# Kernel optimization log

Hardware: AMD Instinct MI355X
Metric: run time of the kernel (lower is better)

Reference implementation:

```python
import jax, jax.numpy as jnp
import numpy as np
from jax import lax

RF, NLF, MESH, FUSION = 64, 16, 16, 64


def _conv3x3(x, w, b):
    # stride 1, pad 1, ksize 3 == SAME
    y = lax.conv_general_dilated(x, w, (1, 1), 'SAME',
                                 dimension_numbers=('NCHW', 'OIHW', 'NCHW'))
    return y + b[None, :, None, None]


def _bn(x, g, b, m, v, eps=1e-5):
    scale = g / jnp.sqrt(v + eps)
    return (x - m[None, :, None, None]) * scale[None, :, None, None] + b[None, :, None, None]


def _rct_block(x, w1, b1, g, be, m, v, w2, b2):
    # extra_conv=True: Conv -> BN -> SiLU -> Conv (all stride 1)
    h = jax.nn.silu(_bn(_conv3x3(x, w1, b1), g, be, m, v))
    return _conv3x3(h, w2, b2)


def setup_inputs():
    key = jax.random.key(0)
    ks = jax.random.split(key, 8)
    B, H, W = 4, 512, 512
    return {
        'feature': jax.random.normal(ks[0], (B, RF, H, W), jnp.float32),
        'p_low': jax.random.normal(ks[1], (B, FUSION, MESH + 1, MESH + 1), jnp.float32),
        'r_w1': jax.random.normal(ks[2], (FUSION, FUSION, 3, 3), jnp.float32) * 0.05,
        'r_b1': jnp.zeros((FUSION,), jnp.float32),
        'r_gamma': jnp.ones((FUSION,), jnp.float32),
        'r_beta': jnp.zeros((FUSION,), jnp.float32),
        'r_mean': jnp.zeros((FUSION,), jnp.float32),
        'r_var': jnp.ones((FUSION,), jnp.float32),
        'r_w2': jax.random.normal(ks[3], (RF * NLF, FUSION, 3, 3), jnp.float32) * 0.05,
        'r_b2': jnp.zeros((RF * NLF,), jnp.float32),
        't_w1': jax.random.normal(ks[4], (FUSION, FUSION, 3, 3), jnp.float32) * 0.05,
        't_b1': jnp.zeros((FUSION,), jnp.float32),
        't_gamma': jnp.ones((FUSION,), jnp.float32),
        't_beta': jnp.zeros((FUSION,), jnp.float32),
        't_mean': jnp.zeros((FUSION,), jnp.float32),
        't_var': jnp.ones((FUSION,), jnp.float32),
        't_w2': jax.random.normal(ks[5], (3 * NLF, FUSION, 3, 3), jnp.float32) * 0.05,
        't_b2': jnp.zeros((3 * NLF,), jnp.float32),
    }


def reference(feature, p_low, r_w1, r_b1, r_gamma, r_beta, r_mean, r_var, r_w2, r_b2,
              t_w1, t_b1, t_gamma, t_beta, t_mean, t_var, t_w2, t_b2):
    B, C, H, W = feature.shape
    M = MESH
    mh, mw = H // M, W // M  # H,W divisible by mesh_size -> pad_tensor is identity
    P = mh * mw

    r_l = _rct_block(p_low, r_w1, r_b1, r_gamma, r_beta, r_mean, r_var, r_w2, r_b2)  # [B, RF*NLF, M+1, M+1]
    t_l = _rct_block(p_low, t_w1, t_b1, t_gamma, t_beta, t_mean, t_var, t_w2, t_b2)  # [B, 3*NLF, M+1, M+1]

    # channel dim factors as (feat, nlf); corners concat along nlf axis in order
    # (i,j), (i,j+1), (i+1,j), (i+1,j+1) -> K = 4*NLF keys per tile
    rc = r_l.reshape(B, RF, NLF, M + 1, M + 1)
    rk = jnp.concatenate([rc[..., :M, :M], rc[..., :M, 1:],
                          rc[..., 1:, :M], rc[..., 1:, 1:]], axis=2)  # [B,RF,4NLF,M,M]
    tc = t_l.reshape(B, 3, NLF, M + 1, M + 1)
    tk = jnp.concatenate([tc[..., :M, :M], tc[..., :M, 1:],
                          tc[..., 1:, :M], tc[..., 1:, 1:]], axis=2)  # [B,3,4NLF,M,M]

    # split feature into tiles: [B, M, M, P, RF] (row-major pixel order within tile)
    f = feature.reshape(B, RF, M, mh, M, mw).transpose(0, 2, 4, 3, 5, 1).reshape(B, M, M, P, RF)

    scale = 1.0 / jnp.sqrt(jnp.float32(RF))
    att = jnp.einsum('bxypr,brkxy->bxypk', f, rk) * scale  # [B,M,M,P,4NLF]
    att = jax.nn.softmax(att, axis=-1)
    out = jnp.einsum('bxypk,bckxy->bxycp', att, tk)  # [B,M,M,3,P]

    Y = out.reshape(B, M, M, 3, mh, mw).transpose(0, 3, 1, 4, 2, 5).reshape(B, 3, H, W)
    return Y
```

## Files before the change

### kernel.cpp

```cpp
#include <hip/hip_runtime.h>

typedef unsigned short u16;
typedef __bf16 bf16x8 __attribute__((ext_vector_type(8)));
typedef unsigned short us8 __attribute__((ext_vector_type(8)));
typedef float f32x4 __attribute__((ext_vector_type(4)));
typedef float f32x2 __attribute__((ext_vector_type(2)));
typedef unsigned int u32x4 __attribute__((ext_vector_type(4)));

union U8u { us8 s; u16 u[8]; };

__device__ __forceinline__ u16 f2bf(float f){
  unsigned u = __builtin_bit_cast(unsigned, f);
  u += 0x7fffu + ((u >> 16) & 1u);
  return (u16)(u >> 16);
}
__device__ __forceinline__ bf16x8 asbf(us8 x){ return __builtin_bit_cast(bf16x8, x); }

#define MFMA16(a,b,c) __builtin_amdgcn_mfma_f32_16x16x32_bf16((a),(b),(c),0,0,0)

__device__ __forceinline__ void stage_zero2(u16* sS, int tid){
  uint* z = (uint*)sS;
  for (int i = tid; i < 12996; i += 256) z[i] = 0u;
}

__device__ __forceinline__ void stage_src_f32T(const float* __restrict__ src,
                                               u16* sS, int tid){
  for (int i4 = tid; i4 < 4624; i4 += 256){
    int e = i4 * 4;
    f32x4 dv = *(const f32x4*)(src + e);
    #pragma unroll
    for (int t = 0; t < 4; t++){
      int ee = e + t;
      int ci = ee / 289; int rr = ee - ci*289;
      int oy = rr / 17;  int ox = rr - oy*17;
      sS[((oy+1)*19 + ox+1)*72 + ci] = f2bf(dv[t]);
    }
  }
}

__device__ __forceinline__ void stage_src_pm(const u16* __restrict__ src,
                                             u16* sS, int tid){
  for (int i8 = tid; i8 < 2312; i8 += 256){
    int pix = i8 >> 3, c0 = (i8 & 7) << 3;
    us8 v = *(const us8*)(src + ((size_t)pix << 6) + c0);
    int oy = pix / 17, ox = pix - oy*17;
    *(us8*)(sS + ((oy+1)*19 + ox+1)*72 + c0) = v;
  }
}

__device__ __forceinline__ void stage_w_f32(const float* __restrict__ w, int m0,
                                            u16* sW, int tid){
  for (int i4 = tid; i4 < 2304; i4 += 256){
    int e = i4 * 4;
    int co = e / 576; int r0 = e - co*576;
    f32x4 wv = *(const f32x4*)(w + (size_t)(m0+co)*576 + r0);
    #pragma unroll
    for (int t = 0; t < 4; t++){
      int r = r0 + t; int cin = r / 9; int tap = r - cin*9;
      sW[co*584 + tap*64 + cin] = f2bf(wv[t]);
    }
  }
}

__device__ __forceinline__ f32x4 conv_tile2(const u16* sS, const u16* sW,
                                            int nt, int l15, int q)
{
  int p = nt*16 + l15; int pc = p > 288 ? 288 : p;
  int oy = pc / 17, ox = pc - oy*17;
  f32x4 acc = {0.f, 0.f, 0.f, 0.f};
  #pragma unroll
  for (int ks = 0; ks < 18; ks++){
    const int tap = ks >> 1;
    const int dy = tap / 3, dx = tap - dy*3;
    int pix2 = (oy+dy)*19 + (ox+dx);
    us8 bv = *(const us8*)(sS + pix2*72 + (ks & 1)*32 + q*8);
    us8 av = *(const us8*)(sW + l15*584 + ks*32 + q*8);
    acc = MFMA16(asbf(av), asbf(bv), acc);
  }
  return acc;
}

__global__ __launch_bounds__(256) void conv1_k(
    const float* __restrict__ p_low,
    const float* __restrict__ wR, const float* __restrict__ b1R,
    const float* __restrict__ gR, const float* __restrict__ beR,
    const float* __restrict__ mR, const float* __restrict__ vR,
    const float* __restrict__ wT, const float* __restrict__ b1T,
    const float* __restrict__ gT, const float* __restrict__ beT,
    const float* __restrict__ mT, const float* __restrict__ vT,
    u16* __restrict__ hR, u16* __restrict__ hT)
{
  __shared__ __attribute__((aligned(16))) u16 sS[25992];
  __shared__ __attribute__((aligned(16))) u16 sW[9344];
  int tid = threadIdx.x;
  int bx = blockIdx.x;
  int job = bx >> 6;
  int b = (bx >> 4) & 3;
  int m0 = ((bx >> 2) & 3) << 4;
  int px = bx & 3;
  int nt0 = px * 5, ntEnd = nt0 + 5 > 19 ? 19 : nt0 + 5;
  const float* w  = job ? wT  : wR;
  const float* b1 = job ? b1T : b1R;
  const float* g  = job ? gT  : gR;
  const float* be = job ? beT : beR;
  const float* mn = job ? mT  : mR;
  const float* vr = job ? vT  : vR;
  u16* out = job ? hT : hR;
  const float* src = p_low + (size_t)b * 18496;

  stage_zero2(sS, tid);
  __syncthreads();
  stage_src_f32T(src, sS, tid);
  stage_w_f32(w, m0, sW, tid);
  __syncthreads();

  int lane = tid & 63, wave = tid >> 6;
  int l15 = lane & 15, q = lane >> 4;
  float scl[4], sft[4];
  #pragma unroll
  for (int e = 0; e < 4; e++){
    int co = m0 + q*4 + e;
    float s = g[co] / sqrtf(vr[co] + 1e-5f);
    scl[e] = s;
    sft[e] = (b1[co] - mn[co]) * s + be[co];
  }
  for (int nt = nt0 + wave; nt < ntEnd; nt += 4){
    f32x4 acc = conv_tile2(sS, sW, nt, l15, q);
    int p = nt*16 + l15;
    if (p < 289){
      float si[4];
      #pragma unroll
      for (int e = 0; e < 4; e++){
        float y = acc[e]*scl[e] + sft[e];
        si[e] = y / (1.f + __expf(-y));
      }
      uint2 pk;
      pk.x = (uint)f2bf(si[0]) | ((uint)f2bf(si[1]) << 16);
      pk.y = (uint)f2bf(si[2]) | ((uint)f2bf(si[3]) << 16);
      *(uint2*)(out + ((size_t)b*289 + p)*64 + m0 + q*4) = pk;
    }
  }
}

__global__ __launch_bounds__(256) void conv2_k(
    const u16* __restrict__ hR, const u16* __restrict__ hT,
    const float* __restrict__ w2R, const float* __restrict__ b2R,
    const float* __restrict__ w2T, const float* __restrict__ b2T,
    u16* __restrict__ rlq, float* __restrict__ tlq)
{
  __shared__ __attribute__((aligned(16))) u16 sS[25992];
  __shared__ __attribute__((aligned(16))) u16 sW[9344];
  int tid = threadIdx.x;
  int bx = blockIdx.x;
  const float *w, *bias; const u16* src;
  int b, m0, isR;
  if (bx < 256){
    isR = 1; b = bx >> 6; m0 = (bx & 63) << 4;
    src = hR + (size_t)b*18496; w = w2R; bias = b2R;
  } else {
    isR = 0; int i = bx - 256; b = i / 3; m0 = (i - b*3) << 4;
    src = hT + (size_t)b*18496; w = w2T; bias = b2T;
  }

  stage_zero2(sS, tid);
  __syncthreads();
  stage_src_pm(src, sS, tid);
  stage_w_f32(w, m0, sW, tid);
  __syncthreads();

  int lane = tid & 63, wave = tid >> 6;
  int l15 = lane & 15, q = lane >> 4;
  float bs[4];
  #pragma unroll
  for (int e = 0; e < 4; e++) bs[e] = bias[m0 + q*4 + e];
  const float PSC = 0.18033688f;
  for (int nt = wave; nt < 19; nt += 4){
    f32x4 acc = conv_tile2(sS, sW, nt, l15, q);
    int p = nt*16 + l15;
    if (p < 289){
      if (isR){
        uint2 pk;
        pk.x = (uint)f2bf((acc[0]+bs[0])*PSC)
             | ((uint)f2bf((acc[1]+bs[1])*PSC) << 16);
        pk.y = (uint)f2bf((acc[2]+bs[2])*PSC)
             | ((uint)f2bf((acc[3]+bs[3])*PSC) << 16);
        *(uint2*)(rlq + ((size_t)b*289 + p)*1024 + m0 + q*4) = pk;
      } else {
        f32x4 ov = {acc[0]+bs[0], acc[1]+bs[1], acc[2]+bs[2], acc[3]+bs[3]};
        *(f32x4*)(tlq + ((size_t)b*289 + p)*48 + m0 + q*4) = ov;
      }
    }
  }
}

__global__ __launch_bounds__(256) void attn_k(
    const uint* __restrict__ feat,
    const u16* __restrict__ rlq, const float* __restrict__ tlq,
    float* __restrict__ out)
{
  __shared__ __attribute__((aligned(16))) u16 rkT[4608];
  __shared__ __attribute__((aligned(16))) float tkF[256];
  int tid = threadIdx.x;
  int ty = blockIdx.x, tx = blockIdx.y, b = blockIdx.z;
  int lane = tid & 63, wave = tid >> 6;
  int l15 = lane & 15, q = lane >> 4;

  {
    int corner = wave;
    int pix = (tx + (corner >> 1))*17 + ty + (corner & 1);
    const u16* sp = rlq + ((size_t)b*289 + pix)*1024 + lane*16;
    U8u v0, v1; v0.s = *(const us8*)sp; v1.s = *(const us8*)(sp + 8);
    #pragma unroll
    for (int nl = 0; nl < 8; nl++){
      rkT[(corner*16 + nl)*72 + lane]     = v0.u[nl];
      rkT[(corner*16 + 8 + nl)*72 + lane] = v1.u[nl];
    }
  }
  if (tid < 192){
    int corner = tid / 48; int idx = tid - corner*48;
    int pix = (tx + (corner >> 1))*17 + ty + (corner & 1);
    int c = idx >> 4, nl = idx & 15;
    tkF[c*64 + corner*16 + nl] = tlq[((size_t)b*289 + pix)*48 + idx];
  }
  __syncthreads();

  bf16x8 frk[4][2];
  #pragma unroll
  for (int nt = 0; nt < 4; nt++)
    #pragma unroll
    for (int ks = 0; ks < 2; ks++)
      frk[nt][ks] = __builtin_bit_cast(bf16x8,
          *(const us8*)(rkT + (nt*16 + l15)*72 + ks*32 + q*8));

  const float* __restrict__ tkq = tkF + q*4;

  const uint HW = 512u*512u;
  const uint* fpb = feat + (size_t)b*64*HW;
  const uint* fb0[8]; const uint* fb1[8];
  #pragma unroll
  for (int j = 0; j < 8; j++){
    fb0[j] = fpb + (size_t)j*HW;
    fb1[j] = fpb + (size_t)(j+32)*HW;
  }
  uint offv = (uint)(q*8)*HW + (uint)(tx*32 + wave*8)*512u + (uint)(ty*32 + l15);

  uint r0[8], r1[8];
  #pragma unroll
  for (int j = 0; j < 8; j++){
    r0[j] = fb0[j][offv];
    r1[j] = fb1[j][offv];
  }

  #pragma unroll
  for (int cnk = 0; cnk < 16; cnk++){
    u32x4 p0v, p1v;
    #pragma unroll
    for (int j2 = 0; j2 < 4; j2++){
      p0v[j2] = __builtin_amdgcn_perm(r0[2*j2+1], r0[2*j2], 0x07060302u);
      p1v[j2] = __builtin_amdgcn_perm(r1[2*j2+1], r1[2*j2], 0x07060302u);
    }
    bf16x8 A0 = __builtin_bit_cast(bf16x8, p0v);
    bf16x8 A1 = __builtin_bit_cast(bf16x8, p1v);

    if (cnk < 15){
      offv += (cnk & 1) ? 496u : 16u;
      #pragma unroll
      for (int j = 0; j < 8; j++){
        r0[j] = fb0[j][offv];
        r1[j] = fb1[j][offv];
      }
    }

    f32x4 acc[4];
    __builtin_amdgcn_s_setprio(1);
    #pragma unroll
    for (int nt = 0; nt < 4; nt++){
      f32x4 zz = {0.f, 0.f, 0.f, 0.f};
      zz = MFMA16(frk[nt][0], A0, zz);
      zz = MFMA16(frk[nt][1], A1, zz);
      acc[nt] = zz;
    }
    __builtin_amdgcn_s_setprio(0);

    f32x2 den2 = {0.f,0.f}, o0v = {0.f,0.f}, o1v = {0.f,0.f}, o2v = {0.f,0.f};
    #pragma unroll
    for (int nt = 0; nt < 4; nt++){
      f32x4 t0 = *(const f32x4*)(tkq + 0*64 + nt*16);
      f32x4 t1 = *(const f32x4*)(tkq + 1*64 + nt*16);
      f32x4 t2 = *(const f32x4*)(tkq + 2*64 + nt*16);
      f32x2 pa, pb;
      pa[0] = __builtin_amdgcn_exp2f(acc[nt][0]);
      pa[1] = __builtin_amdgcn_exp2f(acc[nt][1]);
      pb[0] = __builtin_amdgcn_exp2f(acc[nt][2]);
      pb[1] = __builtin_amdgcn_exp2f(acc[nt][3]);
      den2 += pa; den2 += pb;
      f32x2 t0a = {t0[0], t0[1]}, t0b = {t0[2], t0[3]};
      f32x2 t1a = {t1[0], t1[1]}, t1b = {t1[2], t1[3]};
      f32x2 t2a = {t2[0], t2[1]}, t2b = {t2[2], t2[3]};
      o0v = __builtin_elementwise_fma(pa, t0a, o0v);
      o0v = __builtin_elementwise_fma(pb, t0b, o0v);
      o1v = __builtin_elementwise_fma(pa, t1a, o1v);
      o1v = __builtin_elementwise_fma(pb, t1b, o1v);
      o2v = __builtin_elementwise_fma(pa, t2a, o2v);
      o2v = __builtin_elementwise_fma(pb, t2b, o2v);
    }
    float den = den2[0] + den2[1];
    float o0 = o0v[0] + o0v[1];
    float o1 = o1v[0] + o1v[1];
    float o2 = o2v[0] + o2v[1];
    o0  += __shfl_xor(o0, 16, 64);
    o1  += __shfl_xor(o1, 16, 64);
    o2  += __shfl_xor(o2, 16, 64);
    den += __shfl_xor(den, 16, 64);
    o0  += __shfl_xor(o0, 32, 64);
    o1  += __shfl_xor(o1, 32, 64);
    o2  += __shfl_xor(o2, 32, 64);
    den += __shfl_xor(den, 32, 64);
    float rin = __builtin_amdgcn_rcpf(den);
    float val = (q == 0) ? o0 : ((q == 1) ? o1 : o2);
    int hh = tx*32 + wave*8 + (cnk >> 1);
    int j0 = (cnk & 1) << 4;
    if (q < 3)
      out[((size_t)(b*3 + q)*512 + hh)*512 + (ty*32 + j0 + l15)] = val * rin;
  }
}

extern "C" void kernel_launch(void* const* d_in, const int* in_sizes, int n_in,
                              void* d_out, int out_size, void* d_ws, size_t ws_size,
                              hipStream_t stream)
{
  (void)in_sizes; (void)n_in; (void)out_size; (void)ws_size;
  const uint*  feature = (const uint*)d_in[0];
  const float* p_low = (const float*)d_in[1];
  const float* r_w1 = (const float*)d_in[2];
  const float* r_b1 = (const float*)d_in[3];
  const float* r_g  = (const float*)d_in[4];
  const float* r_be = (const float*)d_in[5];
  const float* r_m  = (const float*)d_in[6];
  const float* r_v  = (const float*)d_in[7];
  const float* r_w2 = (const float*)d_in[8];
  const float* r_b2 = (const float*)d_in[9];
  const float* t_w1 = (const float*)d_in[10];
  const float* t_b1 = (const float*)d_in[11];
  const float* t_g  = (const float*)d_in[12];
  const float* t_be = (const float*)d_in[13];
  const float* t_m  = (const float*)d_in[14];
  const float* t_v  = (const float*)d_in[15];
  const float* t_w2 = (const float*)d_in[16];
  const float* t_b2 = (const float*)d_in[17];

  char* ws = (char*)d_ws;
  u16* hR = (u16*)ws;
  u16* hT = hR + (size_t)4*289*64;
  u16* rlq = (u16*)(ws + 295936);
  float* tlq = (float*)(ws + 295936 + 2367488);
  float* outp = (float*)d_out;

  hipLaunchKernelGGL(conv1_k, dim3(128), dim3(256), 0, stream,
      p_low, r_w1, r_b1, r_g, r_be, r_m, r_v,
      t_w1, t_b1, t_g, t_be, t_m, t_v, hR, hT);
  hipLaunchKernelGGL(conv2_k, dim3(268), dim3(256), 0, stream,
      hR, hT, r_w2, r_b2, t_w2, t_b2, rlq, tlq);
  hipLaunchKernelGGL(attn_k, dim3(16, 16, 4), dim3(256), 0, stream,
      feature, rlq, tlq, outp);
}
```

Before: 446.4 us.

## Stage feature tiles into LDS via global_load_lds with swizzled layout

Replaces per-thread strided global loads of the 64-channel feature tile (one 4-byte load per channel per pixel) with 16-byte global_load_lds transfers into a 32 KB shared buffer, using an XOR swizzle to avoid bank conflicts. Each of the 8 row iterations loads a row slab, synchronizes, then reads A-operands from LDS for two 16-pixel halves. The aim is wider, coalesced DRAM transactions for this bandwidth-bound kernel. In exchange it adds two block barriers per iteration, loses the prior register prefetch overlap and the s_setprio hints, and uses more LDS, which may lower occupancy.

```diff
diff --git a/kernel.cpp b/kernel.cpp
--- a/kernel.cpp
+++ b/kernel.cpp
@@ -200,6 +200,7 @@
 {
   __shared__ __attribute__((aligned(16))) u16 rkT[4608];
   __shared__ __attribute__((aligned(16))) float tkF[256];
+  __shared__ __attribute__((aligned(1024))) uint sF[8192];
   int tid = threadIdx.x;
   int ty = blockIdx.x, tx = blockIdx.y, b = blockIdx.z;
   int lane = tid & 63, wave = tid >> 6;
@@ -234,94 +235,97 @@
 
   const float* __restrict__ tkq = tkF + q*4;
 
-  const uint HW = 512u*512u;
-  const uint* fpb = feat + (size_t)b*64*HW;
-  const uint* fb0[8]; const uint* fb1[8];
-  #pragma unroll
-  for (int j = 0; j < 8; j++){
-    fb0[j] = fpb + (size_t)j*HW;
-    fb1[j] = fpb + (size_t)(j+32)*HW;
-  }
-  uint offv = (uint)(q*8)*HW + (uint)(tx*32 + wave*8)*512u + (uint)(ty*32 + l15);
-
-  uint r0[8], r1[8];
-  #pragma unroll
-  for (int j = 0; j < 8; j++){
-    r0[j] = fb0[j][offv];
-    r1[j] = fb1[j][offv];
-  }
-
-  #pragma unroll
-  for (int cnk = 0; cnk < 16; cnk++){
-    u32x4 p0v, p1v;
-    #pragma unroll
-    for (int j2 = 0; j2 < 4; j2++){
-      p0v[j2] = __builtin_amdgcn_perm(r0[2*j2+1], r0[2*j2], 0x07060302u);
-      p1v[j2] = __builtin_amdgcn_perm(r1[2*j2+1], r1[2*j2], 0x07060302u);
-    }
-    bf16x8 A0 = __builtin_bit_cast(bf16x8, p0v);
-    bf16x8 A1 = __builtin_bit_cast(bf16x8, p1v);
-
-    if (cnk < 15){
-      offv += (cnk & 1) ? 496u : 16u;
+  const size_t HW = (size_t)512*512;
+  int segl = (wave << 3) + (lane >> 3);
+  int part = lane & 7;
+
+  for (int c = 0; c < 8; ++c){
+    #pragma unroll
+    for (int p = 0; p < 8; ++p){
+      int seg = p*32 + segl;
+      int i  = seg >> 6;
+      int ch = seg & 63;
+      int qq = (ch >> 3) & 3;
+      int col0 = ((part ^ (qq << 1)) << 2);
+      const uint* src = feat + ((size_t)(b*64 + ch))*HW
+                      + (size_t)(tx*32 + i*8 + c)*512 + (ty*32 + col0);
+      uint* dst = sF + (size_t)(p*32 + (wave << 3))*32;
+      __builtin_amdgcn_global_load_lds(
+          (const __attribute__((address_space(1))) void*)src,
+          (__attribute__((address_space(3))) void*)dst, 16, 0, 0);
+    }
+    __syncthreads();
+
+    #pragma unroll
+    for (int h = 0; h < 2; ++h){
+      int colL = ((h << 4) + l15) ^ (q << 3);
+      const uint* fp = sF + wave*2048 + q*256 + colL;
+      uint r0[8], r1[8];
       #pragma unroll
       for (int j = 0; j < 8; j++){
-        r0[j] = fb0[j][offv];
-        r1[j] = fb1[j][offv];
-      }
-    }
-
-    f32x4 acc[4];
-    __builtin_amdgcn_s_setprio(1);
-    #pragma unroll
-    for (int nt = 0; nt < 4; nt++){
-      f32x4 zz = {0.f, 0.f, 0.f, 0.f};
-      zz = MFMA16(frk[nt][0], A0, zz);
-      zz = MFMA16(frk[nt][1], A1, zz);
-      acc[nt] = zz;
-    }
-    __builtin_amdgcn_s_setprio(0);
-
-    f32x2 den2 = {0.f,0.f}, o0v = {0.f,0.f}, o1v = {0.f,0.f}, o2v = {0.f,0.f};
-    #pragma unroll
-    for (int nt = 0; nt < 4; nt++){
-      f32x4 t0 = *(const f32x4*)(tkq + 0*64 + nt*16);
-      f32x4 t1 = *(const f32x4*)(tkq + 1*64 + nt*16);
-      f32x4 t2 = *(const f32x4*)(tkq + 2*64 + nt*16);
-      f32x2 pa, pb;
-      pa[0] = __builtin_amdgcn_exp2f(acc[nt][0]);
-      pa[1] = __builtin_amdgcn_exp2f(acc[nt][1]);
-      pb[0] = __builtin_amdgcn_exp2f(acc[nt][2]);
-      pb[1] = __builtin_amdgcn_exp2f(acc[nt][3]);
-      den2 += pa; den2 += pb;
-      f32x2 t0a = {t0[0], t0[1]}, t0b = {t0[2], t0[3]};
-      f32x2 t1a = {t1[0], t1[1]}, t1b = {t1[2], t1[3]};
-      f32x2 t2a = {t2[0], t2[1]}, t2b = {t2[2], t2[3]};
-      o0v = __builtin_elementwise_fma(pa, t0a, o0v);
-      o0v = __builtin_elementwise_fma(pb, t0b, o0v);
-      o1v = __builtin_elementwise_fma(pa, t1a, o1v);
-      o1v = __builtin_elementwise_fma(pb, t1b, o1v);
-      o2v = __builtin_elementwise_fma(pa, t2a, o2v);
-      o2v = __builtin_elementwise_fma(pb, t2b, o2v);
-    }
-    float den = den2[0] + den2[1];
-    float o0 = o0v[0] + o0v[1];
-    float o1 = o1v[0] + o1v[1];
-    float o2 = o2v[0] + o2v[1];
-    o0  += __shfl_xor(o0, 16, 64);
-    o1  += __shfl_xor(o1, 16, 64);
-    o2  += __shfl_xor(o2, 16, 64);
-    den += __shfl_xor(den, 16, 64);
-    o0  += __shfl_xor(o0, 32, 64);
-    o1  += __shfl_xor(o1, 32, 64);
-    o2  += __shfl_xor(o2, 32, 64);
-    den += __shfl_xor(den, 32, 64);
-    float rin = __builtin_amdgcn_rcpf(den);
-    float val = (q == 0) ? o0 : ((q == 1) ? o1 : o2);
-    int hh = tx*32 + wave*8 + (cnk >> 1);
-    int j0 = (cnk & 1) << 4;
-    if (q < 3)
-      out[((size_t)(b*3 + q)*512 + hh)*512 + (ty*32 + j0 + l15)] = val * rin;
+        r0[j] = fp[j*32];
+        r1[j] = fp[1024 + j*32];
+      }
+      u32x4 p0v, p1v;
+      #pragma unroll
+      for (int j2 = 0; j2 < 4; j2++){
+        p0v[j2] = __builtin_amdgcn_perm(r0[2*j2+1], r0[2*j2], 0x07060302u);
+        p1v[j2] = __builtin_amdgcn_perm(r1[2*j2+1], r1[2*j2], 0x07060302u);
+      }
+      bf16x8 A0 = __builtin_bit_cast(bf16x8, p0v);
+      bf16x8 A1 = __builtin_bit_cast(bf16x8, p1v);
+
+      f32x4 acc[4];
+      #pragma unroll
+      for (int nt = 0; nt < 4; nt++){
+        f32x4 zz = {0.f, 0.f, 0.f, 0.f};
+        zz = MFMA16(frk[nt][0], A0, zz);
+        zz = MFMA16(frk[nt][1], A1, zz);
+        acc[nt] = zz;
+      }
+
+      f32x2 den2 = {0.f,0.f}, o0v = {0.f,0.f}, o1v = {0.f,0.f}, o2v = {0.f,0.f};
+      #pragma unroll
+      for (int nt = 0; nt < 4; nt++){
+        f32x4 t0 = *(const f32x4*)(tkq + 0*64 + nt*16);
+        f32x4 t1 = *(const f32x4*)(tkq + 1*64 + nt*16);
+        f32x4 t2 = *(const f32x4*)(tkq + 2*64 + nt*16);
+        f32x2 pa, pb;
+        pa[0] = __builtin_amdgcn_exp2f(acc[nt][0]);
+        pa[1] = __builtin_amdgcn_exp2f(acc[nt][1]);
+        pb[0] = __builtin_amdgcn_exp2f(acc[nt][2]);
+        pb[1] = __builtin_amdgcn_exp2f(acc[nt][3]);
+        den2 += pa; den2 += pb;
+        f32x2 t0a = {t0[0], t0[1]}, t0b = {t0[2], t0[3]};
+        f32x2 t1a = {t1[0], t1[1]}, t1b = {t1[2], t1[3]};
+        f32x2 t2a = {t2[0], t2[1]}, t2b = {t2[2], t2[3]};
+        o0v = __builtin_elementwise_fma(pa, t0a, o0v);
+        o0v = __builtin_elementwise_fma(pb, t0b, o0v);
+        o1v = __builtin_elementwise_fma(pa, t1a, o1v);
+        o1v = __builtin_elementwise_fma(pb, t1b, o1v);
+        o2v = __builtin_elementwise_fma(pa, t2a, o2v);
+        o2v = __builtin_elementwise_fma(pb, t2b, o2v);
+      }
+      float den = den2[0] + den2[1];
+      float o0 = o0v[0] + o0v[1];
+      float o1 = o1v[0] + o1v[1];
+      float o2 = o2v[0] + o2v[1];
+      o0  += __shfl_xor(o0, 16, 64);
+      o1  += __shfl_xor(o1, 16, 64);
+      o2  += __shfl_xor(o2, 16, 64);
+      den += __shfl_xor(den, 16, 64);
+      o0  += __shfl_xor(o0, 32, 64);
+      o1  += __shfl_xor(o1, 32, 64);
+      o2  += __shfl_xor(o2, 32, 64);
+      den += __shfl_xor(den, 32, 64);
+      float rin = __builtin_amdgcn_rcpf(den);
+      float val = (q == 0) ? o0 : ((q == 1) ? o1 : o2);
+      int hh = tx*32 + wave*8 + c;
+      int j0 = h << 4;
+      if (q < 3)
+        out[((size_t)(b*3 + q)*512 + hh)*512 + (ty*32 + j0 + l15)] = val * rin;
+    }
+    __syncthreads();
   }
 }
 
```

After: 442.0 us. Within noise of the previous version (-1.0%).
